# Performance work log

Hardware: AMD Instinct MI355X
Metric: run time of the kernel (lower is better)

The kernel has to match this reference:

```python
import jax, jax.numpy as jnp
import numpy as np

GRID = 1024  # grid resolution -> V = GRID*GRID vertices


def _grid_mesh(G):
    """Build a triangulated GxG grid mesh; return laplacian directed edges and
    normal-consistency interior-edge index quadruples [v0, v1, v2, v3] where
    (v0,v1) is the shared edge and v2, v3 the opposite vertices of the two faces."""
    V = G * G
    i, j = np.meshgrid(np.arange(G - 1), np.arange(G - 1), indexing="ij")
    a = (i * G + j).ravel(); b = (i * G + j + 1).ravel()
    c = ((i + 1) * G + j).ravel(); d = ((i + 1) * G + j + 1).ravel()
    faces = np.concatenate([np.stack([a, b, c], 1), np.stack([b, d, c], 1)], 0).astype(np.int64)
    # half-edges with opposite vertex per face
    e = np.concatenate([faces[:, [0, 1]], faces[:, [1, 2]], faces[:, [2, 0]]], 0)
    opp = np.concatenate([faces[:, 2], faces[:, 0], faces[:, 1]], 0)
    e = np.sort(e, 1)
    key = e[:, 0] * V + e[:, 1]
    order = np.argsort(key, kind="stable")
    ks, opps = key[order], opp[order]
    dup = np.nonzero(ks[1:] == ks[:-1])[0]  # edges shared by exactly two faces
    nc_idx = np.stack([ks[dup] // V, ks[dup] % V, opps[dup], opps[dup + 1]], 1)
    uk = np.unique(key)
    src, dst = uk // V, uk % V
    lap_src = np.concatenate([src, dst])
    lap_dst = np.concatenate([dst, src])
    return lap_src.astype(np.int32), lap_dst.astype(np.int32), nc_idx.astype(np.int32)


def setup_inputs() -> dict:
    key = jax.random.key(0)
    k1, k2 = jax.random.split(key)
    G = GRID; V = G * G
    lap_src, lap_dst, nc_idx = _grid_mesh(G)
    verts = jax.random.normal(k1, (V, 3), jnp.float32)          # template_mesh.verts_packed()
    deform_verts = jax.random.normal(k2, (V, 3), jnp.float32) * 0.05  # nn.Parameter
    return {
        "verts": verts,
        "deform_verts": deform_verts,
        "lap_src": jnp.asarray(lap_src),
        "lap_dst": jnp.asarray(lap_dst),
        "nc_idx": jnp.asarray(nc_idx),
        "batch_size": 4,
    }


def reference(verts, deform_verts, lap_src, lap_dst, nc_idx, batch_size):
    V = verts.shape[0]
    new_verts = verts + deform_verts  # Meshes.offset_verts

    # mesh_laplacian_smoothing(method='uniform'):
    # per-vertex (mean of neighbors - vertex), loss = mean ||.||
    nbr_sum = jax.ops.segment_sum(new_verts[lap_src], lap_dst, num_segments=V)
    deg = jax.ops.segment_sum(jnp.ones(lap_src.shape, jnp.float32), lap_dst, num_segments=V)
    lap = nbr_sum / jnp.maximum(deg, 1.0)[:, None] - new_verts
    laplacian_loss = jnp.linalg.norm(lap, axis=1).mean()

    # mesh_normal_consistency: for each interior edge (v0,v1) with opposite
    # verts v2, v3: n0 = (v1-v0) x (v2-v0), n1 = -(v1-v0) x (v3-v0),
    # loss = mean(1 - cos(n0, n1))
    v0 = new_verts[nc_idx[:, 0]]; v1 = new_verts[nc_idx[:, 1]]
    v2 = new_verts[nc_idx[:, 2]]; v3 = new_verts[nc_idx[:, 3]]
    e01 = v1 - v0
    n0 = jnp.cross(e01, v2 - v0)
    n1 = -jnp.cross(e01, v3 - v0)
    cos = (n0 * n1).sum(-1) / jnp.maximum(
        jnp.linalg.norm(n0, axis=-1) * jnp.linalg.norm(n1, axis=-1), 1e-8)
    flatten_loss = (1.0 - cos).mean()

    # Meshes.extend(batch_size): replicate deformed mesh verts
    batched_verts = jnp.broadcast_to(new_verts, (batch_size, V, 3))
    return batched_verts, laplacian_loss, flatten_loss
```

## Files before the change

### kernel.cpp

```cpp
#include <hip/hip_runtime.h>

#define G 1024
#define ROWF 3072
#define ROWF4 768
#define V (G * G)
#define NBLK 1024
#define COPY4 786432
#define NEDGE 3137541.0f

typedef float v4 __attribute__((ext_vector_type(4)));

struct F3 { float x, y, z; };

__device__ inline F3 ldl(const float* __restrict__ nv, int slot, int col) {
    int b = slot * ROWF + 3 * col;
    F3 r; r.x = nv[b]; r.y = nv[b + 1]; r.z = nv[b + 2];
    return r;
}

__device__ inline float omc(F3 v0, F3 v1, F3 v2, F3 v3) {
    float ex = v1.x - v0.x, ey = v1.y - v0.y, ez = v1.z - v0.z;
    float ax = v2.x - v0.x, ay = v2.y - v0.y, az = v2.z - v0.z;
    float bx = v3.x - v0.x, by = v3.y - v0.y, bz = v3.z - v0.z;
    float n0x = ey * az - ez * ay;
    float n0y = ez * ax - ex * az;
    float n0z = ex * ay - ey * ax;
    float n1x = ez * by - ey * bz;
    float n1y = ex * bz - ez * bx;
    float n1z = ey * bx - ex * by;
    float dd = n0x * n1x + n0y * n1y + n0z * n1z;
    float m0 = sqrtf(n0x * n0x + n0y * n0y + n0z * n0z);
    float m1 = sqrtf(n1x * n1x + n1y * n1y + n1z * n1z);
    float c  = dd / fmaxf(m0 * m1, 1e-8f);
    return 1.0f - c;
}

__global__ __launch_bounds__(256) void fused_kernel(const float* __restrict__ verts,
                                                    const float* __restrict__ dv,
                                                    float* __restrict__ out,
                                                    float* __restrict__ wsp) {
    int b = blockIdx.x;
    int i = ((b & 7) << 7) | (b >> 3);
    int t = threadIdx.x;

    __shared__ v4 nv4[3 * ROWF4];
    const float* nv = (const float*)nv4;

    const v4* vin4 = (const v4*)verts;
    const v4* dvi4 = (const v4*)dv;

    #pragma unroll
    for (int s = 0; s < 3; ++s) {
        int r = i + s - 1;
        r = r < 0 ? 0 : (r > G - 1 ? G - 1 : r);
        int base = r * ROWF4;
        #pragma unroll
        for (int k = 0; k < 3; ++k) {
            int idx = t + (k << 8);
            nv4[s * ROWF4 + idx] = vin4[base + idx] + dvi4[base + idx];
        }
    }
    __syncthreads();

    bool hasU = (i > 0), hasD = (i < G - 1);

    v4* out4 = (v4*)out;
    #pragma unroll
    for (int k = 0; k < 3; ++k) {
        int idx = t + (k << 8);
        v4 val  = nv4[ROWF4 + idx];
        int oi  = i * ROWF4 + idx;
        __builtin_nontemporal_store(val, &out4[oi]);
        __builtin_nontemporal_store(val, &out4[oi + COPY4]);
        __builtin_nontemporal_store(val, &out4[oi + 2 * COPY4]);
        __builtin_nontemporal_store(val, &out4[oi + 3 * COPY4]);
    }

    float lap_sum = 0.0f, fl_sum = 0.0f;

    #pragma unroll
    for (int k = 0; k < 4; ++k) {
        int j = t + (k << 8);
        bool hasL = (j > 0), hasR = (j < G - 1);

        F3 self = ldl(nv, 1, j);
        F3 pL{0,0,0}, pR{0,0,0}, pU{0,0,0}, pD{0,0,0}, pUR{0,0,0}, pDL{0,0,0}, pDR{0,0,0};
        if (hasL)          pL  = ldl(nv, 1, j - 1);
        if (hasR)          pR  = ldl(nv, 1, j + 1);
        if (hasU)          pU  = ldl(nv, 0, j);
        if (hasD)          pD  = ldl(nv, 2, j);
        if (hasU && hasR)  pUR = ldl(nv, 0, j + 1);
        if (hasD && hasL)  pDL = ldl(nv, 2, j - 1);
        if (hasD && hasR)  pDR = ldl(nv, 2, j + 1);

        int   degi = (int)hasL + (int)hasR + (int)hasU + (int)hasD
                   + (int)(hasU && hasR) + (int)(hasD && hasL);
        float inv  = 1.0f / (float)degi;
        float lx = (pL.x + pR.x + pU.x + pD.x + pUR.x + pDL.x) * inv - self.x;
        float ly = (pL.y + pR.y + pU.y + pD.y + pUR.y + pDL.y) * inv - self.y;
        float lz = (pL.z + pR.z + pU.z + pD.z + pUR.z + pDL.z) * inv - self.z;
        lap_sum += sqrtf(lx * lx + ly * ly + lz * lz);

        if (hasD && hasR) {
            fl_sum += omc(pR, pD, self, pDR);
            if (hasU) fl_sum += omc(self, pR, pD, pUR);
            if (hasL) fl_sum += omc(self, pD, pR, pDL);
        }
    }

    for (int off = 32; off > 0; off >>= 1) {
        lap_sum += __shfl_down(lap_sum, off);
        fl_sum  += __shfl_down(fl_sum, off);
    }
    __shared__ float red[8];
    int lane = t & 63, wv = t >> 6;
    if (lane == 0) { red[wv] = lap_sum; red[4 + wv] = fl_sum; }
    __syncthreads();
    if (t == 0) {
        wsp[b]        = red[0] + red[1] + red[2] + red[3];
        wsp[NBLK + b] = red[4] + red[5] + red[6] + red[7];
    }
}

__global__ __launch_bounds__(256) void finalize_kernel(const float* __restrict__ wsp,
                                                       float* __restrict__ out) {
    float s = 0.0f, f = 0.0f;
    for (int k = threadIdx.x; k < NBLK; k += 256) {
        s += wsp[k];
        f += wsp[NBLK + k];
    }
    for (int off = 32; off > 0; off >>= 1) {
        s += __shfl_down(s, off);
        f += __shfl_down(f, off);
    }
    __shared__ float red[8];
    int lane = threadIdx.x & 63, wv = threadIdx.x >> 6;
    if (lane == 0) { red[wv] = s; red[4 + wv] = f; }
    __syncthreads();
    if (threadIdx.x == 0) {
        out[12 * V]     = (red[0] + red[1] + red[2] + red[3]) / (float)V;
        out[12 * V + 1] = (red[4] + red[5] + red[6] + red[7]) / NEDGE;
    }
}

extern "C" void kernel_launch(void* const* d_in, const int* in_sizes, int n_in,
                              void* d_out, int out_size, void* d_ws, size_t ws_size,
                              hipStream_t stream) {
    const float* verts = (const float*)d_in[0];
    const float* dv    = (const float*)d_in[1];
    float* out = (float*)d_out;
    float* wsp = (float*)d_ws;

    fused_kernel<<<NBLK, 256, 0, stream>>>(verts, dv, out, wsp);
    finalize_kernel<<<1, 256, 0, stream>>>(wsp, out);
}
```

Baseline: 156.0 us.

## Fuse finalize via last-block ticket, register-blocked stencil with interior fast path

Drops the separate finalize launch: each block bumps a global ticket after writing its partials, and the last block to arrive does the final reduction. The stencil now gives each thread 4 contiguous columns, loaded as vector LDS reads into registers. Padded LDS slots provide the halo, and interior threads take a branch-free path with a constant degree of 6. Fast hardware sqrt/rcp intrinsics and a launch-bounds occupancy hint are also added. This adds an atomic and fences, and slightly lowers the precision of the cosine terms.

```diff
diff --git a/kernel.cpp b/kernel.cpp
--- a/kernel.cpp
+++ b/kernel.cpp
@@ -1,20 +1,24 @@
 #include <hip/hip_runtime.h>
 
 #define G 1024
-#define ROWF 3072
 #define ROWF4 768
 #define V (G * G)
 #define NBLK 1024
 #define COPY4 786432
 #define NEDGE 3137541.0f
+#define SLOTF4 773
 
 typedef float v4 __attribute__((ext_vector_type(4)));
 
 struct F3 { float x, y, z; };
 
-__device__ inline F3 ldl(const float* __restrict__ nv, int slot, int col) {
-    int b = slot * ROWF + 3 * col;
-    F3 r; r.x = nv[b]; r.y = nv[b + 1]; r.z = nv[b + 2];
+__device__ inline F3 vc(const float* b, int r) {
+    F3 p; p.x = b[3 * r + 1]; p.y = b[3 * r + 2]; p.z = b[3 * r + 3];
+    return p;
+}
+
+__device__ inline F3 sel(bool c, F3 a) {
+    F3 r; r.x = c ? a.x : 0.0f; r.y = c ? a.y : 0.0f; r.z = c ? a.z : 0.0f;
     return r;
 }
 
@@ -29,22 +33,22 @@
     float n1y = ex * bz - ez * bx;
     float n1z = ey * bx - ex * by;
     float dd = n0x * n1x + n0y * n1y + n0z * n1z;
-    float m0 = sqrtf(n0x * n0x + n0y * n0y + n0z * n0z);
-    float m1 = sqrtf(n1x * n1x + n1y * n1y + n1z * n1z);
-    float c  = dd / fmaxf(m0 * m1, 1e-8f);
-    return 1.0f - c;
+    float m0 = __builtin_amdgcn_sqrtf(n0x * n0x + n0y * n0y + n0z * n0z);
+    float m1 = __builtin_amdgcn_sqrtf(n1x * n1x + n1y * n1y + n1z * n1z);
+    return 1.0f - dd * __builtin_amdgcn_rcpf(fmaxf(m0 * m1, 1e-8f));
 }
 
-__global__ __launch_bounds__(256) void fused_kernel(const float* __restrict__ verts,
-                                                    const float* __restrict__ dv,
-                                                    float* __restrict__ out,
-                                                    float* __restrict__ wsp) {
+__device__ unsigned int g_ticket = 0;
+
+__global__ __launch_bounds__(256, 4) void fused_kernel(const float* __restrict__ verts,
+                                                       const float* __restrict__ dv,
+                                                       float* __restrict__ out,
+                                                       float* __restrict__ wsp) {
     int b = blockIdx.x;
     int i = ((b & 7) << 7) | (b >> 3);
     int t = threadIdx.x;
 
-    __shared__ v4 nv4[3 * ROWF4];
-    const float* nv = (const float*)nv4;
+    __shared__ v4 nv4[3 * SLOTF4];
 
     const v4* vin4 = (const v4*)verts;
     const v4* dvi4 = (const v4*)dv;
@@ -57,18 +61,16 @@
         #pragma unroll
         for (int k = 0; k < 3; ++k) {
             int idx = t + (k << 8);
-            nv4[s * ROWF4 + idx] = vin4[base + idx] + dvi4[base + idx];
+            nv4[s * SLOTF4 + 1 + idx] = vin4[base + idx] + dvi4[base + idx];
         }
     }
     __syncthreads();
-
-    bool hasU = (i > 0), hasD = (i < G - 1);
 
     v4* out4 = (v4*)out;
     #pragma unroll
     for (int k = 0; k < 3; ++k) {
         int idx = t + (k << 8);
-        v4 val  = nv4[ROWF4 + idx];
+        v4 val  = nv4[SLOTF4 + 1 + idx];
         int oi  = i * ROWF4 + idx;
         __builtin_nontemporal_store(val, &out4[oi]);
         __builtin_nontemporal_store(val, &out4[oi + COPY4]);
@@ -76,35 +78,66 @@
         __builtin_nontemporal_store(val, &out4[oi + 3 * COPY4]);
     }
 
+    float bu[20], bm[20], bd[20];
+    #pragma unroll
+    for (int q = 0; q < 5; ++q) {
+        v4 a = nv4[0 * SLOTF4 + 3 * t + q];
+        v4 c = nv4[1 * SLOTF4 + 3 * t + q];
+        v4 d = nv4[2 * SLOTF4 + 3 * t + q];
+        bu[4*q] = a.x; bu[4*q+1] = a.y; bu[4*q+2] = a.z; bu[4*q+3] = a.w;
+        bm[4*q] = c.x; bm[4*q+1] = c.y; bm[4*q+2] = c.z; bm[4*q+3] = c.w;
+        bd[4*q] = d.x; bd[4*q+1] = d.y; bd[4*q+2] = d.z; bd[4*q+3] = d.w;
+    }
+
     float lap_sum = 0.0f, fl_sum = 0.0f;
 
-    #pragma unroll
-    for (int k = 0; k < 4; ++k) {
-        int j = t + (k << 8);
-        bool hasL = (j > 0), hasR = (j < G - 1);
+    if (i > 0 && i < G - 1 && t > 0 && t < 255) {
+        #pragma unroll
+        for (int rc = 1; rc <= 4; ++rc) {
+            F3 self = vc(bm, rc);
+            F3 pL  = vc(bm, rc - 1), pR  = vc(bm, rc + 1);
+            F3 pU  = vc(bu, rc),     pD  = vc(bd, rc);
+            F3 pUR = vc(bu, rc + 1), pDL = vc(bd, rc - 1), pDR = vc(bd, rc + 1);
 
-        F3 self = ldl(nv, 1, j);
-        F3 pL{0,0,0}, pR{0,0,0}, pU{0,0,0}, pD{0,0,0}, pUR{0,0,0}, pDL{0,0,0}, pDR{0,0,0};
-        if (hasL)          pL  = ldl(nv, 1, j - 1);
-        if (hasR)          pR  = ldl(nv, 1, j + 1);
-        if (hasU)          pU  = ldl(nv, 0, j);
-        if (hasD)          pD  = ldl(nv, 2, j);
-        if (hasU && hasR)  pUR = ldl(nv, 0, j + 1);
-        if (hasD && hasL)  pDL = ldl(nv, 2, j - 1);
-        if (hasD && hasR)  pDR = ldl(nv, 2, j + 1);
+            const float inv6 = 1.0f / 6.0f;
+            float lx = (pL.x + pR.x + pU.x + pD.x + pUR.x + pDL.x) * inv6 - self.x;
+            float ly = (pL.y + pR.y + pU.y + pD.y + pUR.y + pDL.y) * inv6 - self.y;
+            float lz = (pL.z + pR.z + pU.z + pD.z + pUR.z + pDL.z) * inv6 - self.z;
+            lap_sum += __builtin_amdgcn_sqrtf(lx * lx + ly * ly + lz * lz);
 
-        int   degi = (int)hasL + (int)hasR + (int)hasU + (int)hasD
-                   + (int)(hasU && hasR) + (int)(hasD && hasL);
-        float inv  = 1.0f / (float)degi;
-        float lx = (pL.x + pR.x + pU.x + pD.x + pUR.x + pDL.x) * inv - self.x;
-        float ly = (pL.y + pR.y + pU.y + pD.y + pUR.y + pDL.y) * inv - self.y;
-        float lz = (pL.z + pR.z + pU.z + pD.z + pUR.z + pDL.z) * inv - self.z;
-        lap_sum += sqrtf(lx * lx + ly * ly + lz * lz);
+            fl_sum += omc(pR, pD, self, pDR);
+            fl_sum += omc(self, pR, pD, pUR);
+            fl_sum += omc(self, pD, pR, pDL);
+        }
+    } else {
+        bool hasU = (i > 0), hasD = (i < G - 1);
+        #pragma unroll
+        for (int rc = 1; rc <= 4; ++rc) {
+            int j = 4 * t + rc - 1;
+            bool hasL = (j > 0), hasR = (j < G - 1);
 
-        if (hasD && hasR) {
-            fl_sum += omc(pR, pD, self, pDR);
-            if (hasU) fl_sum += omc(self, pR, pD, pUR);
-            if (hasL) fl_sum += omc(self, pD, pR, pDL);
+            F3 self = vc(bm, rc);
+            F3 pL  = sel(hasL, vc(bm, rc - 1));
+            F3 pR  = sel(hasR, vc(bm, rc + 1));
+            F3 pU  = sel(hasU, vc(bu, rc));
+            F3 pD  = sel(hasD, vc(bd, rc));
+            F3 pUR = sel(hasU && hasR, vc(bu, rc + 1));
+            F3 pDL = sel(hasD && hasL, vc(bd, rc - 1));
+            F3 pDR = sel(hasD && hasR, vc(bd, rc + 1));
+
+            int   degi = (int)hasL + (int)hasR + (int)hasU + (int)hasD
+                       + (int)(hasU && hasR) + (int)(hasD && hasL);
+            float inv  = 1.0f / (float)degi;
+            float lx = (pL.x + pR.x + pU.x + pD.x + pUR.x + pDL.x) * inv - self.x;
+            float ly = (pL.y + pR.y + pU.y + pD.y + pUR.y + pDL.y) * inv - self.y;
+            float lz = (pL.z + pR.z + pU.z + pD.z + pUR.z + pDL.z) * inv - self.z;
+            lap_sum += __builtin_amdgcn_sqrtf(lx * lx + ly * ly + lz * lz);
+
+            if (hasD && hasR) {
+                fl_sum += omc(pR, pD, self, pDR);
+                if (hasU) fl_sum += omc(self, pR, pD, pUR);
+                if (hasL) fl_sum += omc(self, pD, pR, pDL);
+            }
         }
     }
 
@@ -113,33 +146,38 @@
         fl_sum  += __shfl_down(fl_sum, off);
     }
     __shared__ float red[8];
+    __shared__ unsigned int lastflag;
     int lane = t & 63, wv = t >> 6;
     if (lane == 0) { red[wv] = lap_sum; red[4 + wv] = fl_sum; }
     __syncthreads();
+
     if (t == 0) {
         wsp[b]        = red[0] + red[1] + red[2] + red[3];
         wsp[NBLK + b] = red[4] + red[5] + red[6] + red[7];
+        __threadfence();
+        unsigned int tk = atomicAdd(&g_ticket, 1u);
+        lastflag = (tk == NBLK - 1u) ? 1u : 0u;
+        if (lastflag) atomicExch(&g_ticket, 0u);
     }
-}
+    __syncthreads();
 
-__global__ __launch_bounds__(256) void finalize_kernel(const float* __restrict__ wsp,
-                                                       float* __restrict__ out) {
-    float s = 0.0f, f = 0.0f;
-    for (int k = threadIdx.x; k < NBLK; k += 256) {
-        s += wsp[k];
-        f += wsp[NBLK + k];
-    }
-    for (int off = 32; off > 0; off >>= 1) {
-        s += __shfl_down(s, off);
-        f += __shfl_down(f, off);
-    }
-    __shared__ float red[8];
-    int lane = threadIdx.x & 63, wv = threadIdx.x >> 6;
-    if (lane == 0) { red[wv] = s; red[4 + wv] = f; }
-    __syncthreads();
-    if (threadIdx.x == 0) {
-        out[12 * V]     = (red[0] + red[1] + red[2] + red[3]) / (float)V;
-        out[12 * V + 1] = (red[4] + red[5] + red[6] + red[7]) / NEDGE;
+    if (lastflag) {
+        __threadfence();
+        float s = 0.0f, f = 0.0f;
+        for (int k = t; k < NBLK; k += 256) {
+            s += wsp[k];
+            f += wsp[NBLK + k];
+        }
+        for (int off = 32; off > 0; off >>= 1) {
+            s += __shfl_down(s, off);
+            f += __shfl_down(f, off);
+        }
+        if (lane == 0) { red[wv] = s; red[4 + wv] = f; }
+        __syncthreads();
+        if (t == 0) {
+            out[12 * V]     = (red[0] + red[1] + red[2] + red[3]) / (float)V;
+            out[12 * V + 1] = (red[4] + red[5] + red[6] + red[7]) / NEDGE;
+        }
     }
 }
 
@@ -152,5 +190,4 @@
     float* wsp = (float*)d_ws;
 
     fused_kernel<<<NBLK, 256, 0, stream>>>(verts, dv, out, wsp);
-    finalize_kernel<<<1, 256, 0, stream>>>(wsp, out);
 }
```

After: 197.6 us. 26.7% more time.
